# Performance work log

Measured on AMD Instinct MI355X. Metric: run time of the kernel, lower is better.

The kernel has to match this reference:

```python
import jax, jax.numpy as jnp
import numpy as np

N = 100000        # number of nodes
E = 1600000       # number of edges (avg degree 16)
D_IN = 512
D_OUT = 64


def setup_inputs() -> dict:
    key = jax.random.key(0)
    k1, k2, k3, k4, k5 = jax.random.split(key, 5)
    inputs = jax.random.normal(k1, (N, D_IN), dtype=jnp.float32)
    weight = jax.random.normal(k2, (D_IN, D_OUT), dtype=jnp.float32)
    adj_vals = jax.random.uniform(k3, (E,), dtype=jnp.float32)
    adj_rows = jax.random.randint(k4, (E,), 0, N, dtype=jnp.int32)
    adj_cols = jax.random.randint(k5, (E,), 0, N, dtype=jnp.int32)
    return {
        "inputs": inputs,
        "weight": weight,
        "adj_vals": adj_vals,
        "adj_rows": adj_rows,
        "adj_cols": adj_cols,
    }


def reference(inputs, weight, adj_vals, adj_rows, adj_cols):
    # Dense projection: [N, D_IN] @ [D_IN, D_OUT] -> [N, D_OUT]
    h = inputs @ weight
    # Sparse adjacency spmm (COO): out[r] += vals[e] * h[c] for edge e=(r,c)
    msgs = adj_vals[:, None] * h[adj_cols]            # [E, D_OUT]
    agg = jax.ops.segment_sum(msgs, adj_rows, num_segments=N)  # [N, D_OUT]
    # activation = relu
    return jax.nn.relu(agg)
```

## Files before the change

kernel.cpp:

```cpp
#include <hip/hip_runtime.h>
#include <hip/hip_bf16.h>

#define D_OUT 64
#define K_DIM 512
#define RPB 128
#define RPB_SHIFT 7
#define EPB 8192
#define RCAP 3072

using short8  = __attribute__((ext_vector_type(8))) short;
using floatx4 = __attribute__((ext_vector_type(4))) float;

__device__ inline unsigned short f32_to_bf16(float f) {
    unsigned int u = __float_as_uint(f);
    u += 0x7FFFu + ((u >> 16) & 1u);
    return (unsigned short)(u >> 16);
}

__global__ void wt_kernel(const float* __restrict__ W, unsigned short* __restrict__ wt) {
    int i = blockIdx.x * blockDim.x + threadIdx.x;
    if (i < D_OUT * K_DIM) {
        int n = i >> 9;
        int k = i & 511;
        wt[i] = f32_to_bf16(W[k * D_OUT + n]);
    }
}

__global__ __launch_bounds__(256) void gemm_kernel(
    const float* __restrict__ A, const unsigned short* __restrict__ wt,
    float* __restrict__ H, int n) {
    const int tid  = threadIdx.x;
    const int wv   = tid >> 6;
    const int lane = tid & 63;
    const int ln   = lane & 15;
    const int quad = lane >> 4;
    const int row0 = blockIdx.x * 64 + wv * 16;

    int arow = row0 + ln;
    if (arow >= n) arow = n - 1;
    const float* Arow = A + (size_t)arow * K_DIM;
    const unsigned short* wb = wt + (size_t)ln * K_DIM;

    floatx4 acc0 = {0.f, 0.f, 0.f, 0.f};
    floatx4 acc1 = {0.f, 0.f, 0.f, 0.f};
    floatx4 acc2 = {0.f, 0.f, 0.f, 0.f};
    floatx4 acc3 = {0.f, 0.f, 0.f, 0.f};

    for (int h0 = 0; h0 < K_DIM; h0 += 128) {
        float4 t[8];
#pragma unroll
        for (int s = 0; s < 4; s++) {
            t[2 * s]     = *reinterpret_cast<const float4*>(Arow + h0 + s * 32 + quad * 8);
            t[2 * s + 1] = *reinterpret_cast<const float4*>(Arow + h0 + s * 32 + quad * 8 + 4);
        }
        short8 ab[4];
#pragma unroll
        for (int s = 0; s < 4; s++) {
            float4 a0 = t[2 * s], a1 = t[2 * s + 1];
            short8 af;
            af[0] = (short)f32_to_bf16(a0.x);
            af[1] = (short)f32_to_bf16(a0.y);
            af[2] = (short)f32_to_bf16(a0.z);
            af[3] = (short)f32_to_bf16(a0.w);
            af[4] = (short)f32_to_bf16(a1.x);
            af[5] = (short)f32_to_bf16(a1.y);
            af[6] = (short)f32_to_bf16(a1.z);
            af[7] = (short)f32_to_bf16(a1.w);
            ab[s] = af;
        }
#pragma unroll
        for (int s = 0; s < 4; s++) {
            const int ko = h0 + s * 32 + quad * 8;
            short8 b0 = *reinterpret_cast<const short8*>(wb + ko);
            short8 b1 = *reinterpret_cast<const short8*>(wb + 16 * K_DIM + ko);
            short8 b2 = *reinterpret_cast<const short8*>(wb + 32 * K_DIM + ko);
            short8 b3 = *reinterpret_cast<const short8*>(wb + 48 * K_DIM + ko);
            acc0 = __builtin_amdgcn_mfma_f32_16x16x32_bf16(ab[s], b0, acc0, 0, 0, 0);
            acc1 = __builtin_amdgcn_mfma_f32_16x16x32_bf16(ab[s], b1, acc1, 0, 0, 0);
            acc2 = __builtin_amdgcn_mfma_f32_16x16x32_bf16(ab[s], b2, acc2, 0, 0, 0);
            acc3 = __builtin_amdgcn_mfma_f32_16x16x32_bf16(ab[s], b3, acc3, 0, 0, 0);
        }
    }

#pragma unroll
    for (int r = 0; r < 4; r++) {
        int gr = row0 + quad * 4 + r;
        if (gr < n) {
            float* Hr = H + (size_t)gr * D_OUT;
            Hr[ln]      = acc0[r];
            Hr[16 + ln] = acc1[r];
            Hr[32 + ln] = acc2[r];
            Hr[48 + ln] = acc3[r];
        }
    }
}

__global__ __launch_bounds__(256) void count_kernel(
    const int* __restrict__ rows, int* __restrict__ counts,
    int E, int nbuck, int nb) {
    extern __shared__ int cnt[];
    const int tid = threadIdx.x, blk = blockIdx.x;
    for (int b = tid; b < nbuck; b += 256) cnt[b] = 0;
    __syncthreads();
    const int base = blk * EPB;
#pragma unroll
    for (int i = 0; i < EPB / 256; i++) {
        int e = base + tid + i * 256;
        if (e < E) atomicAdd(&cnt[rows[e] >> RPB_SHIFT], 1);
    }
    __syncthreads();
    for (int b = tid; b < nbuck; b += 256) counts[b * nb + blk] = cnt[b];
}

__global__ __launch_bounds__(256) void scan1_kernel(
    const int* __restrict__ counts, int* __restrict__ bsum, int n) {
    __shared__ int wsh[4];
    const int tid = threadIdx.x, lane = tid & 63, wid = tid >> 6;
    int i0 = blockIdx.x * 1024 + tid * 4;
    int s = 0;
#pragma unroll
    for (int j = 0; j < 4; j++) {
        int ix = i0 + j;
        s += (ix < n) ? counts[ix] : 0;
    }
#pragma unroll
    for (int d = 32; d; d >>= 1) s += __shfl_xor(s, d, 64);
    if (lane == 0) wsh[wid] = s;
    __syncthreads();
    if (tid == 0) bsum[blockIdx.x] = wsh[0] + wsh[1] + wsh[2] + wsh[3];
}

__global__ __launch_bounds__(1024) void scan2_kernel(
    const int* __restrict__ bsum, int* __restrict__ bbase,
    int* __restrict__ scanned, int nblk, int L, int E) {
    __shared__ int wsum[16];
    const int tid = threadIdx.x, lane = tid & 63, wid = tid >> 6;
    int v = (tid < nblk) ? bsum[tid] : 0;
    int x = v;
#pragma unroll
    for (int d = 1; d < 64; d <<= 1) {
        int y = __shfl_up(x, d, 64);
        if (lane >= d) x += y;
    }
    if (lane == 63) wsum[wid] = x;
    __syncthreads();
    if (tid < 16) {
        int w = wsum[tid];
        int xx = w;
#pragma unroll
        for (int d = 1; d < 16; d <<= 1) {
            int y = __shfl_up(xx, d, 64);
            if (tid >= d) xx += y;
        }
        wsum[tid] = xx - w;
    }
    __syncthreads();
    if (tid < nblk) bbase[tid] = wsum[wid] + (x - v);
    if (tid == 0) scanned[L] = E;
}

__global__ __launch_bounds__(256) void scan3_kernel(
    const int* __restrict__ counts, const int* __restrict__ bbase,
    int* __restrict__ scanned, int n) {
    __shared__ int wsum[4];
    const int tid = threadIdx.x, lane = tid & 63, wid = tid >> 6;
    const int i0 = blockIdx.x * 1024 + tid * 4;
    int v[4];
#pragma unroll
    for (int j = 0; j < 4; j++) {
        int ix = i0 + j;
        v[j] = (ix < n) ? counts[ix] : 0;
    }
#pragma unroll
    for (int j = 1; j < 4; j++) v[j] += v[j - 1];
    int t = v[3];
    int x = t;
#pragma unroll
    for (int d = 1; d < 64; d <<= 1) {
        int y = __shfl_up(x, d, 64);
        if (lane >= d) x += y;
    }
    if (lane == 63) wsum[wid] = x;
    __syncthreads();
    if (tid == 0) {
        int a = 0;
#pragma unroll
        for (int w = 0; w < 4; w++) { int tmp = wsum[w]; wsum[w] = a; a += tmp; }
    }
    __syncthreads();
    int excl = bbase[blockIdx.x] + wsum[wid] + (x - t);
#pragma unroll
    for (int j = 0; j < 4; j++) {
        int ix = i0 + j;
        if (ix < n) scanned[ix] = excl + ((j == 0) ? 0 : v[j - 1]);
    }
}

__global__ __launch_bounds__(256) void partition_kernel(
    const int* __restrict__ rows, const int* __restrict__ cols,
    const float* __restrict__ vals, const int* __restrict__ scanned,
    int2* __restrict__ keys, int E, int nbuck, int nb) {
    extern __shared__ int offs[];
    const int tid = threadIdx.x, blk = blockIdx.x;
    for (int b = tid; b < nbuck; b += 256) offs[b] = scanned[b * nb + blk];
    __syncthreads();
    const int base = blk * EPB;
#pragma unroll
    for (int i = 0; i < EPB / 256; i++) {
        int e = base + tid + i * 256;
        if (e < E) {
            int r = rows[e];
            int c = cols[e];
            float v = vals[e];
            int b = r >> RPB_SHIFT;
            int p = atomicAdd(&offs[b], 1);
            keys[p] = make_int2(c | ((r & (RPB - 1)) << 17), __float_as_int(v));
        }
    }
}

__global__ __launch_bounds__(512) void sort_agg_kernel(
    const float* __restrict__ h, const int2* __restrict__ keys,
    const int* __restrict__ scanned, float* __restrict__ out,
    int N, int nb) {
    __shared__ int2 rec[RCAP];
    __shared__ int cnt[RPB];
    __shared__ int excl[RPB];
    __shared__ int cur[RPB];
    __shared__ int wtot[2];

    const int tid  = threadIdx.x;
    const int lane = tid & 63;
    const int wv   = tid >> 6;
    const int b    = blockIdx.x;

    const int start = scanned[b * nb];
    const int end   = scanned[(b + 1) * nb];
    const int m     = end - start;

    if (tid < RPB) cnt[tid] = 0;
    __syncthreads();

    for (int i = tid; i < m; i += 512) {
        int rl = keys[start + i].x >> 17;
        atomicAdd(&cnt[rl], 1);
    }
    __syncthreads();

    int v = 0, x = 0;
    if (tid < RPB) {
        v = cnt[tid];
        x = v;
#pragma unroll
        for (int d = 1; d < 64; d <<= 1) {
            int y = __shfl_up(x, d, 64);
            if (lane >= d) x += y;
        }
        if (lane == 63) wtot[tid >> 6] = x;
    }
    __syncthreads();
    if (tid < RPB) {
        int base = (tid >= 64) ? wtot[0] : 0;
        int ex = base + x - v;
        excl[tid] = ex;
        cur[tid]  = ex;
    }
    __syncthreads();

    for (int i = tid; i < m; i += 512) {
        int2 kv = keys[start + i];
        int rl = kv.x >> 17;
        int p = atomicAdd(&cur[rl], 1);
        if (p < RCAP) rec[p] = kv;
    }
    __syncthreads();

    const int row0 = b * RPB;
    for (int rl = wv; rl < RPB; rl += 8) {
        int s = excl[rl];
        int e = cur[rl];
        float acc = 0.f;
        int j = s;
        for (; j + 4 <= e; j += 4) {
            int2 k0 = rec[j], k1 = rec[j + 1], k2 = rec[j + 2], k3 = rec[j + 3];
            float g0 = h[(size_t)(k0.x & 0x1FFFF) * D_OUT + lane];
            float g1 = h[(size_t)(k1.x & 0x1FFFF) * D_OUT + lane];
            float g2 = h[(size_t)(k2.x & 0x1FFFF) * D_OUT + lane];
            float g3 = h[(size_t)(k3.x & 0x1FFFF) * D_OUT + lane];
            acc += __int_as_float(k0.y) * g0;
            acc += __int_as_float(k1.y) * g1;
            acc += __int_as_float(k2.y) * g2;
            acc += __int_as_float(k3.y) * g3;
        }
        for (; j < e; j++) {
            int2 kv = rec[j];
            acc += __int_as_float(kv.y) * h[(size_t)(kv.x & 0x1FFFF) * D_OUT + lane];
        }
        int gr = row0 + rl;
        if (gr < N) out[(size_t)gr * D_OUT + lane] = fmaxf(acc, 0.f);
    }
}

extern "C" void kernel_launch(void* const* d_in, const int* in_sizes, int n_in,
                              void* d_out, int out_size, void* d_ws, size_t ws_size,
                              hipStream_t stream) {
    const float* A    = (const float*)d_in[0];
    const float* W    = (const float*)d_in[1];
    const float* vals = (const float*)d_in[2];
    const int*   rows = (const int*)d_in[3];
    const int*   cols = (const int*)d_in[4];
    float* out = (float*)d_out;

    const int N = out_size / D_OUT;
    const int E = in_sizes[2];
    const int nbuck = (N + RPB - 1) >> RPB_SHIFT;
    const int nb = (E + EPB - 1) / EPB;
    const int L = nbuck * nb;
    const int SB = (L + 1023) / 1024;

    char* ws = (char*)d_ws;
    float*          h       = (float*)ws;
    int2*           keys    = (int2*)(ws + (size_t)N * D_OUT * 4);
    unsigned short* wt      = (unsigned short*)((char*)keys + (size_t)E * 8);
    int*            counts  = (int*)((char*)wt + (size_t)D_OUT * K_DIM * 2);
    int*            scanned = counts + L;
    int*            bsum    = scanned + L + 1;
    int*            bbase   = bsum + SB;

    const size_t cnt_lds = (size_t)nbuck * 4;

    wt_kernel<<<(D_OUT * K_DIM + 255) / 256, 256, 0, stream>>>(W, wt);
    gemm_kernel<<<(N + 63) / 64, 256, 0, stream>>>(A, wt, h, N);
    count_kernel<<<nb, 256, cnt_lds, stream>>>(rows, counts, E, nbuck, nb);
    scan1_kernel<<<SB, 256, 0, stream>>>(counts, bsum, L);
    scan2_kernel<<<1, 1024, 0, stream>>>(bsum, bbase, scanned, SB, L, E);
    scan3_kernel<<<SB, 256, 0, stream>>>(counts, bbase, scanned, L);
    partition_kernel<<<nb, 256, cnt_lds, stream>>>(rows, cols, vals, scanned, keys, E, nbuck, nb);
    sort_agg_kernel<<<nbuck, 512, 0, stream>>>(h, keys, scanned, out, N, nb);
}
```

Measured before the change: 436.5 us.

## Store projected features as bf16 and gather four edges per wavefront

The GEMM output h is now written as bf16 instead of fp32, which halves the footprint of the intermediate and the bytes moved by the random row gathers in the aggregation. The aggregation loop is restructured so each quarter-wave handles a different edge, with each lane loading four bf16 values via 8-byte loads. Partial sums are combined with cross-lane shuffles before a float4 store. This adds an extra bf16 rounding of h, which could reduce accuracy, and adds shuffle reduction overhead per output row.

```diff
diff --git a/kernel.cpp b/kernel.cpp
--- a/kernel.cpp
+++ b/kernel.cpp
@@ -17,6 +17,13 @@
     return (unsigned short)(u >> 16);
 }
 
+__device__ inline float bf16lo_f32(unsigned int g) {
+    return __uint_as_float(g << 16);
+}
+__device__ inline float bf16hi_f32(unsigned int g) {
+    return __uint_as_float(g & 0xFFFF0000u);
+}
+
 __global__ void wt_kernel(const float* __restrict__ W, unsigned short* __restrict__ wt) {
     int i = blockIdx.x * blockDim.x + threadIdx.x;
     if (i < D_OUT * K_DIM) {
@@ -28,7 +35,7 @@
 
 __global__ __launch_bounds__(256) void gemm_kernel(
     const float* __restrict__ A, const unsigned short* __restrict__ wt,
-    float* __restrict__ H, int n) {
+    unsigned short* __restrict__ H, int n) {
     const int tid  = threadIdx.x;
     const int wv   = tid >> 6;
     const int lane = tid & 63;
@@ -86,11 +93,11 @@
     for (int r = 0; r < 4; r++) {
         int gr = row0 + quad * 4 + r;
         if (gr < n) {
-            float* Hr = H + (size_t)gr * D_OUT;
-            Hr[ln]      = acc0[r];
-            Hr[16 + ln] = acc1[r];
-            Hr[32 + ln] = acc2[r];
-            Hr[48 + ln] = acc3[r];
+            unsigned short* Hr = H + (size_t)gr * D_OUT;
+            Hr[ln]      = f32_to_bf16(acc0[r]);
+            Hr[16 + ln] = f32_to_bf16(acc1[r]);
+            Hr[32 + ln] = f32_to_bf16(acc2[r]);
+            Hr[48 + ln] = f32_to_bf16(acc3[r]);
         }
     }
 }
@@ -220,7 +227,7 @@
 }
 
 __global__ __launch_bounds__(512) void sort_agg_kernel(
-    const float* __restrict__ h, const int2* __restrict__ keys,
+    const unsigned short* __restrict__ h, const int2* __restrict__ keys,
     const int* __restrict__ scanned, float* __restrict__ out,
     int N, int nb) {
     __shared__ int2 rec[RCAP];
@@ -232,6 +239,8 @@
     const int tid  = threadIdx.x;
     const int lane = tid & 63;
     const int wv   = tid >> 6;
+    const int q    = lane >> 4;
+    const int li   = lane & 15;
     const int b    = blockIdx.x;
 
     const int start = scanned[b * nb];
@@ -279,25 +288,55 @@
     for (int rl = wv; rl < RPB; rl += 8) {
         int s = excl[rl];
         int e = cur[rl];
-        float acc = 0.f;
+        float4 acc = {0.f, 0.f, 0.f, 0.f};
         int j = s;
-        for (; j + 4 <= e; j += 4) {
-            int2 k0 = rec[j], k1 = rec[j + 1], k2 = rec[j + 2], k3 = rec[j + 3];
-            float g0 = h[(size_t)(k0.x & 0x1FFFF) * D_OUT + lane];
-            float g1 = h[(size_t)(k1.x & 0x1FFFF) * D_OUT + lane];
-            float g2 = h[(size_t)(k2.x & 0x1FFFF) * D_OUT + lane];
-            float g3 = h[(size_t)(k3.x & 0x1FFFF) * D_OUT + lane];
-            acc += __int_as_float(k0.y) * g0;
-            acc += __int_as_float(k1.y) * g1;
-            acc += __int_as_float(k2.y) * g2;
-            acc += __int_as_float(k3.y) * g3;
-        }
-        for (; j < e; j++) {
-            int2 kv = rec[j];
-            acc += __int_as_float(kv.y) * h[(size_t)(kv.x & 0x1FFFF) * D_OUT + lane];
-        }
+        for (; j + 8 <= e; j += 8) {
+            int2 kA = rec[j + q];
+            int2 kB = rec[j + 4 + q];
+            const uint2 gA = *reinterpret_cast<const uint2*>(
+                h + (size_t)(kA.x & 0x1FFFF) * D_OUT + li * 4);
+            const uint2 gB = *reinterpret_cast<const uint2*>(
+                h + (size_t)(kB.x & 0x1FFFF) * D_OUT + li * 4);
+            float vA = __int_as_float(kA.y);
+            float vB = __int_as_float(kB.y);
+            acc.x += vA * bf16lo_f32(gA.x);
+            acc.y += vA * bf16hi_f32(gA.x);
+            acc.z += vA * bf16lo_f32(gA.y);
+            acc.w += vA * bf16hi_f32(gA.y);
+            acc.x += vB * bf16lo_f32(gB.x);
+            acc.y += vB * bf16hi_f32(gB.x);
+            acc.z += vB * bf16lo_f32(gB.y);
+            acc.w += vB * bf16hi_f32(gB.y);
+        }
+        for (; j < e; j += 4) {
+            bool on = (j + q) < e;
+            int2 kv = rec[on ? j + q : j];
+            const uint2 g = *reinterpret_cast<const uint2*>(
+                h + (size_t)(kv.x & 0x1FFFF) * D_OUT + li * 4);
+            float vv = on ? __int_as_float(kv.y) : 0.f;
+            acc.x += vv * bf16lo_f32(g.x);
+            acc.y += vv * bf16hi_f32(g.x);
+            acc.z += vv * bf16lo_f32(g.y);
+            acc.w += vv * bf16hi_f32(g.y);
+        }
+        acc.x += __shfl_xor(acc.x, 16, 64);
+        acc.y += __shfl_xor(acc.y, 16, 64);
+        acc.z += __shfl_xor(acc.z, 16, 64);
+        acc.w += __shfl_xor(acc.w, 16, 64);
+        acc.x += __shfl_xor(acc.x, 32, 64);
+        acc.y += __shfl_xor(acc.y, 32, 64);
+        acc.z += __shfl_xor(acc.z, 32, 64);
+        acc.w += __shfl_xor(acc.w, 32, 64);
+
         int gr = row0 + rl;
-        if (gr < N) out[(size_t)gr * D_OUT + lane] = fmaxf(acc, 0.f);
+        if (gr < N && q == 0) {
+            float4 o;
+            o.x = fmaxf(acc.x, 0.f);
+            o.y = fmaxf(acc.y, 0.f);
+            o.z = fmaxf(acc.z, 0.f);
+            o.w = fmaxf(acc.w, 0.f);
+            *reinterpret_cast<float4*>(out + (size_t)gr * D_OUT + li * 4) = o;
+        }
     }
 }
 
@@ -319,8 +358,8 @@
     const int SB = (L + 1023) / 1024;
 
     char* ws = (char*)d_ws;
-    float*          h       = (float*)ws;
-    int2*           keys    = (int2*)(ws + (size_t)N * D_OUT * 4);
+    unsigned short* h       = (unsigned short*)ws;
+    int2*           keys    = (int2*)(ws + (size_t)N * D_OUT * 2);
     unsigned short* wt      = (unsigned short*)((char*)keys + (size_t)E * 8);
     int*            counts  = (int*)((char*)wt + (size_t)D_OUT * K_DIM * 2);
     int*            scanned = counts + L;
```

After: 412.4 us. 5.5% less time.
